# Performance work log

Hardware: AMD Instinct MI355X
Metric: run time of the kernel (lower is better)

The kernel has to match this reference:

```python
import jax, jax.numpy as jnp
import numpy as np

N_HEAD = 12


def setup_inputs() -> dict:
    key = jax.random.key(0)
    k1, k2, k3 = jax.random.split(key, 3)
    B, T, C = 1, 4096, 768
    x = jax.random.normal(k1, (B, T, C), dtype=jnp.float32)
    w_attn = jax.random.normal(k2, (C, 3 * C), dtype=jnp.float32) * (1.0 / np.sqrt(C))
    w_proj = jax.random.normal(k3, (C, C), dtype=jnp.float32) * (1.0 / np.sqrt(C))
    return {"x": x, "w_attn": w_attn, "w_proj": w_proj}


def reference(x, w_attn, w_proj):
    B, T, C = x.shape
    hd = C // N_HEAD
    qkv = x @ w_attn  # [B, T, 3C]
    q, k, v = jnp.split(qkv, 3, axis=-1)
    # [B, H, T, hd]
    q = q.reshape(B, T, N_HEAD, hd).transpose(0, 2, 1, 3)
    k = k.reshape(B, T, N_HEAD, hd).transpose(0, 2, 1, 3)
    v = v.reshape(B, T, N_HEAD, hd).transpose(0, 2, 1, 3)
    scale = 1.0 / np.sqrt(hd).astype(np.float32)
    att = jnp.einsum('bhtd,bhsd->bhts', q, k) * scale  # materialized TxT scores
    causal = jnp.tril(jnp.ones((T, T), dtype=bool))
    att = jnp.where(causal[None, None], att, -jnp.inf)
    att = jax.nn.softmax(att, axis=-1)
    y = jnp.einsum('bhts,bhsd->bhtd', att, v)  # [B, H, T, hd]
    y = y.transpose(0, 2, 1, 3).reshape(B, T, C)
    return y @ w_proj
```

## Files before the change

### kernel.cpp

```cpp
#include <hip/hip_runtime.h>


typedef short bf16x8 __attribute__((ext_vector_type(8)));
typedef float f32x4 __attribute__((ext_vector_type(4)));

#define T_SEQ 4096
#define C_DIM 768
#define NH 12
#define HD 64

__device__ __forceinline__ unsigned short f2bf(float f) {
  union { float f; unsigned u; } v; v.f = f;
  unsigned r = v.u + 0x7FFFu + ((v.u >> 16) & 1u);
  return (unsigned short)(r >> 16);
}
__device__ __forceinline__ float bf2f(unsigned short u) {
  union { unsigned u; float f; } v; v.u = ((unsigned)u) << 16;
  return v.f;
}
__device__ __forceinline__ unsigned cvtpk(float a, float b) {
  unsigned r;
  asm("v_cvt_pk_bf16_f32 %0, %1, %2" : "=v"(r) : "v"(a), "v"(b));
  return r;
}
#define E2(x) __builtin_amdgcn_exp2f(x)

#define GLD16(g, l) __builtin_amdgcn_global_load_lds( \
    (const __attribute__((address_space(1))) void*)(g), \
    (__attribute__((address_space(3))) void*)(l), 16, 0, 0)

__device__ __forceinline__ void tr_body(const float* __restrict__ in,
                                        unsigned short* __restrict__ out,
                                        int R, int Cc, int bx, int by,
                                        float (*tile)[33]) {
  int tx = threadIdx.x & 31, ty = threadIdx.x >> 5;
#pragma unroll
  for (int i = 0; i < 32; i += 8)
    tile[ty + i][tx] = in[(size_t)(by * 32 + ty + i) * Cc + bx * 32 + tx];
  __syncthreads();
#pragma unroll
  for (int i = 0; i < 32; i += 8)
    out[(size_t)(bx * 32 + ty + i) * R + by * 32 + tx] = f2bf(tile[tx][ty + i]);
}

__global__ void prep(const float* __restrict__ x, unsigned short* __restrict__ Xb,
                     const float* __restrict__ w_attn, unsigned short* __restrict__ WaT,
                     const float* __restrict__ w_proj, unsigned short* __restrict__ WpT) {
  __shared__ float tile[32][33];
  const int bid = blockIdx.x;
  if (bid < 3072) {
    int i = (bid * 256 + threadIdx.x) * 4;
    float4 v = *reinterpret_cast<const float4*>(x + i);
    ushort4 o;
    o.x = f2bf(v.x); o.y = f2bf(v.y); o.z = f2bf(v.z); o.w = f2bf(v.w);
    *reinterpret_cast<ushort4*>(Xb + i) = o;
  } else if (bid < 3072 + 1728) {
    int b = bid - 3072;
    tr_body(w_attn, WaT, 768, 2304, b % 72, b / 72, tile);
  } else {
    int b = bid - 4800;
    tr_body(w_proj, WpT, 768, 768, b % 24, b / 24, tile);
  }
}

template <int MODE>
__global__ __launch_bounds__(256, 4)
void gemm_bt(const unsigned short* __restrict__ A,
             const unsigned short* __restrict__ Bt,
             void* __restrict__ out0,
             unsigned short* __restrict__ Kout,
             unsigned short* __restrict__ Vt,
             int M, int N, int K) {
  __shared__ __align__(16) unsigned short As[128 * 64];
  __shared__ __align__(16) unsigned short Bs[64 * 64];
  const int nbn = N / 64;
  const int nwg = (M / 128) * nbn;
  const int cpx = nwg >> 3;
  const int swz = ((int)blockIdx.x & 7) * cpx + ((int)blockIdx.x >> 3);
  const int bm = swz / nbn, bn = swz % nbn;
  const int tid = threadIdx.x;
  const int wid = tid >> 6, lane = tid & 63;
  const int wr = wid >> 1, wc = wid & 1;
  const int lr = lane & 15;
  const int lk8 = (lane >> 4) * 8;
  const int rsub = lane >> 3, csub = (lane & 7) * 8;

  f32x4 acc[4][2] = {};

  const int nk = K / 64;
  for (int kt = 0; kt < nk; ++kt) {
    __syncthreads();
    {
      const unsigned short* gA = A + (size_t)(bm * 128) * K + kt * 64;
      const unsigned short* gB = Bt + (size_t)(bn * 64) * K + kt * 64;
#pragma unroll
      for (int c = 0; c < 4; ++c) {
        int seg = wid * 4 + c;
        int row = seg * 8 + rsub;
        GLD16(gA + (size_t)row * K + csub, (char*)As + seg * 1024);
      }
#pragma unroll
      for (int c = 0; c < 2; ++c) {
        int seg = wid * 2 + c;
        int row = seg * 8 + rsub;
        GLD16(gB + (size_t)row * K + csub, (char*)Bs + seg * 1024);
      }
    }
    __syncthreads();
#pragma unroll
    for (int kk = 0; kk < 2; ++kk) {
      bf16x8 a[4], b[2];
      int lk = kk * 32 + lk8;
#pragma unroll
      for (int m = 0; m < 4; ++m)
        a[m] = *reinterpret_cast<const bf16x8*>(&As[(wr * 64 + m * 16 + lr) * 64 + lk]);
#pragma unroll
      for (int n = 0; n < 2; ++n)
        b[n] = *reinterpret_cast<const bf16x8*>(&Bs[(wc * 32 + n * 16 + lr) * 64 + lk]);
#pragma unroll
      for (int m = 0; m < 4; ++m)
#pragma unroll
        for (int n = 0; n < 2; ++n)
          acc[m][n] = __builtin_amdgcn_mfma_f32_16x16x32_bf16(a[m], b[n], acc[m][n], 0, 0, 0);
    }
  }

  const int row0 = bm * 128 + wr * 64;
  const int col0 = bn * 64 + wc * 32;
#pragma unroll
  for (int m = 0; m < 4; ++m)
#pragma unroll
    for (int n = 0; n < 2; ++n)
#pragma unroll
      for (int j = 0; j < 4; ++j) {
        int r = row0 + m * 16 + (lane >> 4) * 4 + j;
        int c = col0 + n * 16 + (lane & 15);
        float v = acc[m][n][j];
        if (MODE == 0) {
          if (c < 768)
            ((unsigned short*)out0)[(size_t)r * 768 + c] = f2bf(v * 0.180336884f);
          else if (c < 1536)
            Kout[(size_t)r * 768 + (c - 768)] = f2bf(v);
          else
            Vt[(size_t)(c - 1536) * M + r] = f2bf(v);
        } else {
          ((float*)out0)[(size_t)r * N + c] = v;
        }
      }
}

__device__ __forceinline__ void stage_kv(const unsigned short* __restrict__ Kb,
                                         const unsigned short* __restrict__ Vt,
                                         unsigned short* Kbuf, unsigned short* Vbuf,
                                         int h, int st, int wid, int lane) {
  const int cg = lane & 7, rsub = (lane >> 3) & 7;
  const unsigned short* gK = Kb + (size_t)(st * 64) * C_DIM + h * 64;
  const unsigned short* gV = Vt + (size_t)(h * 64) * T_SEQ + st * 64;
#pragma unroll
  for (int c = 0; c < 2; ++c) {
    int seg = wid * 2 + c;
    int row = seg * 8 + rsub;
    GLD16(gK + (size_t)row * C_DIM + (cg ^ rsub) * 8, (char*)Kbuf + seg * 1024);
    GLD16(gV + (size_t)row * T_SEQ + (cg ^ rsub) * 8, (char*)Vbuf + seg * 1024);
  }
}

__device__ __forceinline__ int nchunks(int q) { return (2 * q + 13) / 12; }
__device__ __forceinline__ int part_off(int qb) {
  if (qb < 12) return (qb - 6) * 2;
  if (qb < 18) return 12 + (qb - 12) * 3;
  if (qb < 24) return 30 + (qb - 18) * 4;
  if (qb < 30) return 54 + (qb - 24) * 5;
  return 84 + (qb - 30) * 6;
}
__device__ __forceinline__ unsigned short* part_ptr(char* pA, char* pB, int set) {
  return (set < 768) ? (unsigned short*)(pA + (size_t)set * 16384)
                     : (unsigned short*)(pB + (size_t)(set - 768) * 16384);
}

__global__ __launch_bounds__(256, 3)
void attn_fwd(const unsigned short* __restrict__ Qb,
              const unsigned short* __restrict__ Kb,
              const unsigned short* __restrict__ Vt,
              unsigned short* __restrict__ Y,
              char* __restrict__ partA, char* __restrict__ partB,
              float* __restrict__ ml) {
  __shared__ __align__(16) unsigned short Ks[2][64 * 64];
  __shared__ __align__(16) unsigned short Vs[2][64 * 64];
  __shared__ __align__(16) unsigned short Ps[4][32 * 64];

  const int h = blockIdx.x;
  int qb = 0, ck = 0;
  {
    int idx = blockIdx.y;
    for (int q = 31; q >= 0; --q) {
      int nc = nchunks(q);
      if (idx < nc) { qb = q; ck = idx; break; }
      idx -= nc;
    }
  }
  const int nch = nchunks(qb);
  const int q0 = qb * 128;
  const int nst_total = 2 * qb + 2;
  const int st0 = ck * 12;
  const int st1 = (st0 + 12 < nst_total) ? st0 + 12 : nst_total;

  const int tid = threadIdx.x;
  const int wid = tid >> 6, lane = tid & 63;
  const int l15 = lane & 15, g = lane >> 4;
  const int sw = l15 & 7;
  const int qw = q0 + wid * 32;

  bf16x8 qf[2][2];
#pragma unroll
  for (int m = 0; m < 2; ++m)
#pragma unroll
    for (int kk = 0; kk < 2; ++kk)
      qf[m][kk] = *reinterpret_cast<const bf16x8*>(
          &Qb[(size_t)(qw + m * 16 + l15) * C_DIM + h * 64 + kk * 32 + g * 8]);

  f32x4 o[2][4] = {};
  float mrow[2] = {-1e30f, -1e30f};
  float lsum[2] = {0.f, 0.f};

  stage_kv(Kb, Vt, Ks[0], Vs[0], h, st0, wid, lane);
  int cur = 0;

  for (int st = st0; st < st1; ++st) {
    if (st + 1 < st1) {
      stage_kv(Kb, Vt, Ks[cur ^ 1], Vs[cur ^ 1], h, st + 1, wid, lane);
      asm volatile("s_waitcnt vmcnt(4)" ::: "memory");
    } else {
      asm volatile("s_waitcnt vmcnt(0)" ::: "memory");
    }
    __builtin_amdgcn_s_barrier();

    const bool active = (st * 64) <= (qw + 31);
    if (active) {
      const unsigned short* K_ = Ks[cur];
      const unsigned short* V_ = Vs[cur];

      f32x4 sT[2][4] = {};
      __builtin_amdgcn_s_setprio(1);
#pragma unroll
      for (int kk = 0; kk < 2; ++kk) {
        bf16x8 kf[4];
#pragma unroll
        for (int n = 0; n < 4; ++n)
          kf[n] = *reinterpret_cast<const bf16x8*>(
              &K_[(n * 16 + l15) * 64 + (((kk * 4 + g) ^ sw) * 8)]);
#pragma unroll
        for (int m = 0; m < 2; ++m)
#pragma unroll
          for (int n = 0; n < 4; ++n)
            sT[m][n] = __builtin_amdgcn_mfma_f32_16x16x32_bf16(kf[n], qf[m][kk], sT[m][n], 0, 0, 0);
      }
      __builtin_amdgcn_s_setprio(0);

      unsigned short* Pw = Ps[wid];
#pragma unroll
      for (int m = 0; m < 2; ++m) {
        if (!(st * 64 + 63 <= qw + m * 16)) {
          const int bound = (qw + m * 16 + l15) - st * 64;
#pragma unroll
          for (int n = 0; n < 4; ++n)
#pragma unroll
            for (int jj = 0; jj < 4; ++jj) {
              int sl = n * 16 + g * 4 + jj;
              if (sl > bound) sT[m][n][jj] = -1e30f;
            }
        }
        float vm[4];
#pragma unroll
        for (int n = 0; n < 4; ++n)
          vm[n] = fmaxf(fmaxf(sT[m][n][0], sT[m][n][1]), fmaxf(sT[m][n][2], sT[m][n][3]));
        float vmax = fmaxf(fmaxf(vm[0], vm[1]), fmaxf(vm[2], vm[3]));
        vmax = fmaxf(vmax, __shfl_xor(vmax, 16, 64));
        vmax = fmaxf(vmax, __shfl_xor(vmax, 32, 64));
        const bool defer = (__all(vmax <= mrow[m] + 8.0f) != 0);
        const float mnew = defer ? mrow[m] : fmaxf(mrow[m], vmax);
#pragma unroll
        for (int n = 0; n < 4; ++n)
#pragma unroll
          for (int jj = 0; jj < 4; ++jj)
            sT[m][n][jj] = E2(sT[m][n][jj] - mnew);
        float sm[4];
#pragma unroll
        for (int n = 0; n < 4; ++n)
          sm[n] = (sT[m][n][0] + sT[m][n][1]) + (sT[m][n][2] + sT[m][n][3]);
        float ps = (sm[0] + sm[1]) + (sm[2] + sm[3]);
        ps += __shfl_xor(ps, 16, 64);
        ps += __shfl_xor(ps, 32, 64);
        if (defer) {
          lsum[m] += ps;
        } else {
          float alpha = E2(mrow[m] - mnew);
          lsum[m] = lsum[m] * alpha + ps;
          mrow[m] = mnew;
#pragma unroll
          for (int n2 = 0; n2 < 4; ++n2) o[m][n2] *= alpha;
        }
#pragma unroll
        for (int n = 0; n < 4; ++n) {
          uint2 pw;
          pw.x = cvtpk(sT[m][n][0], sT[m][n][1]);
          pw.y = cvtpk(sT[m][n][2], sT[m][n][3]);
          *reinterpret_cast<uint2*>(
              &Pw[(m * 16 + l15) * 64 + (((n * 2 + (g >> 1)) ^ sw) * 8) + (g & 1) * 4]) = pw;
        }
      }
      asm volatile("s_waitcnt lgkmcnt(0)" ::: "memory");

      __builtin_amdgcn_s_setprio(1);
#pragma unroll
      for (int ks = 0; ks < 2; ++ks) {
        bf16x8 vf[4], pf[2];
#pragma unroll
        for (int n2 = 0; n2 < 4; ++n2)
          vf[n2] = *reinterpret_cast<const bf16x8*>(
              &V_[(n2 * 16 + l15) * 64 + (((ks * 4 + g) ^ sw) * 8)]);
#pragma unroll
        for (int m = 0; m < 2; ++m)
          pf[m] = *reinterpret_cast<const bf16x8*>(
              &Pw[(m * 16 + l15) * 64 + (((ks * 4 + g) ^ sw) * 8)]);
#pragma unroll
        for (int m = 0; m < 2; ++m)
#pragma unroll
          for (int n2 = 0; n2 < 4; ++n2)
            o[m][n2] = __builtin_amdgcn_mfma_f32_16x16x32_bf16(vf[n2], pf[m], o[m][n2], 0, 0, 0);
      }
      __builtin_amdgcn_s_setprio(0);
    }
    asm volatile("" ::: "memory");
    __builtin_amdgcn_s_barrier();
    cur ^= 1;
  }

  if (nch == 1) {
#pragma unroll
    for (int m = 0; m < 2; ++m) {
      float inv = 1.0f / lsum[m];
      int qg = qw + m * 16 + l15;
#pragma unroll
      for (int n2 = 0; n2 < 4; ++n2) {
        uint2 yk;
        yk.x = cvtpk(o[m][n2][0] * inv, o[m][n2][1] * inv);
        yk.y = cvtpk(o[m][n2][2] * inv, o[m][n2][3] * inv);
        *reinterpret_cast<uint2*>(&Y[(size_t)qg * C_DIM + h * 64 + n2 * 16 + g * 4]) = yk;
      }
    }
  } else {
    const int set = h * 96 + part_off(qb) + ck;
    unsigned short* po = part_ptr(partA, partB, set);
#pragma unroll
    for (int m = 0; m < 2; ++m) {
      int qL = wid * 32 + m * 16 + l15;
#pragma unroll
      for (int n2 = 0; n2 < 4; ++n2) {
        uint2 pk;
        pk.x = cvtpk(o[m][n2][0], o[m][n2][1]);
        pk.y = cvtpk(o[m][n2][2], o[m][n2][3]);
        *reinterpret_cast<uint2*>(&po[qL * 64 + n2 * 16 + g * 4]) = pk;
      }
      if (g == 0) {
        ml[(size_t)set * 256 + qL * 2] = mrow[m];
        ml[(size_t)set * 256 + qL * 2 + 1] = lsum[m];
      }
    }
  }
}

__global__ __launch_bounds__(256)
void attn_combine(char* __restrict__ partA, char* __restrict__ partB,
                  const float* __restrict__ ml, unsigned short* __restrict__ Y) {
  const int qb = 6 + blockIdx.x;
  const int h = blockIdx.y;
  const int nch = nchunks(qb);
  const int set0 = h * 96 + part_off(qb);
  const int t = threadIdx.x;
  const int r = t >> 1, dh = (t & 1) * 32;

  float mi[6], li[6];
  float M = -1e30f;
  for (int i = 0; i < nch; ++i) {
    mi[i] = ml[(size_t)(set0 + i) * 256 + r * 2];
    li[i] = ml[(size_t)(set0 + i) * 256 + r * 2 + 1];
    M = fmaxf(M, mi[i]);
  }
  float L = 0.f;
  float O[32];
#pragma unroll
  for (int d = 0; d < 32; ++d) O[d] = 0.f;
  for (int i = 0; i < nch; ++i) {
    float w = E2(mi[i] - M);
    L += li[i] * w;
    const unsigned short* po = part_ptr(partA, partB, set0 + i) + r * 64 + dh;
#pragma unroll
    for (int d4 = 0; d4 < 32; d4 += 4) {
      ushort4 v = *reinterpret_cast<const ushort4*>(po + d4);
      O[d4 + 0] += bf2f(v.x) * w;
      O[d4 + 1] += bf2f(v.y) * w;
      O[d4 + 2] += bf2f(v.z) * w;
      O[d4 + 3] += bf2f(v.w) * w;
    }
  }
  float inv = 1.0f / L;
  unsigned short* yp = Y + (size_t)(qb * 128 + r) * C_DIM + h * 64 + dh;
#pragma unroll
  for (int d4 = 0; d4 < 32; d4 += 4) {
    uint2 yk;
    yk.x = cvtpk(O[d4 + 0] * inv, O[d4 + 1] * inv);
    yk.y = cvtpk(O[d4 + 2] * inv, O[d4 + 3] * inv);
    *reinterpret_cast<uint2*>(yp + d4) = yk;
  }
}

extern "C" void kernel_launch(void* const* d_in, const int* in_sizes, int n_in,
                              void* d_out, int out_size, void* d_ws, size_t ws_size,
                              hipStream_t stream) {
  const float* x = (const float*)d_in[0];
  const float* w_attn = (const float*)d_in[1];
  const float* w_proj = (const float*)d_in[2];
  float* out = (float*)d_out;

  char* ws = (char*)d_ws;
  unsigned short* Xb   = (unsigned short*)(ws + 0);
  unsigned short* WaT  = (unsigned short*)(ws + 6291456);
  unsigned short* WpT  = (unsigned short*)(ws + 9830400);
  unsigned short* Qb   = (unsigned short*)(ws + 11010048);
  unsigned short* Kb   = (unsigned short*)(ws + 17301504);
  unsigned short* Vt   = (unsigned short*)(ws + 23592960);
  unsigned short* Yb   = (unsigned short*)(ws + 29884416);

  char* partA = (char*)d_out;
  char* partB = (char*)ws;
  float* mlp  = (float*)(ws + 6291456);

  prep<<<5376, 256, 0, stream>>>(x, Xb, w_attn, WaT, w_proj, WpT);

  gemm_bt<0><<<(T_SEQ / 128) * (2304 / 64), 256, 0, stream>>>(
      Xb, WaT, (void*)Qb, Kb, Vt, T_SEQ, 2304, C_DIM);

  attn_fwd<<<dim3(NH, 102), 256, 0, stream>>>(Qb, Kb, Vt, Yb, partA, partB, mlp);
  attn_combine<<<dim3(26, NH), 256, 0, stream>>>(partA, partB, mlp, Yb);

  gemm_bt<1><<<(T_SEQ / 128) * (C_DIM / 64), 256, 0, stream>>>(
      Yb, WpT, (void*)out, nullptr, nullptr, T_SEQ, C_DIM, C_DIM);
}
```

Before: 138.1 us.

## Single-buffer V tile in attention and shrink output-projection GEMM tile

The attention kernel now double-buffers only K, keeps one V buffer, and issues the next V load after the end-of-iteration barrier. This cuts LDS use, which may allow more resident workgroups. In exchange, the V load has less time to arrive before the PV MFMAs need it. The GEMM is templated on tile size, and the output projection uses 64x64 tiles to launch twice as many workgroups, trading per-block reuse for better occupancy across the CUs.

```diff
diff --git a/kernel.cpp b/kernel.cpp
--- a/kernel.cpp
+++ b/kernel.cpp
@@ -63,7 +63,7 @@
   }
 }
 
-template <int MODE>
+template <int MODE, int BM, int BN>
 __global__ __launch_bounds__(256, 4)
 void gemm_bt(const unsigned short* __restrict__ A,
              const unsigned short* __restrict__ Bt,
@@ -71,10 +71,11 @@
              unsigned short* __restrict__ Kout,
              unsigned short* __restrict__ Vt,
              int M, int N, int K) {
-  __shared__ __align__(16) unsigned short As[128 * 64];
-  __shared__ __align__(16) unsigned short Bs[64 * 64];
-  const int nbn = N / 64;
-  const int nwg = (M / 128) * nbn;
+  __shared__ __align__(16) unsigned short As[BM * 64];
+  __shared__ __align__(16) unsigned short Bs[BN * 64];
+  constexpr int AM = BM / 32, AN = BN / 32;
+  const int nbn = N / BN;
+  const int nwg = (M / BM) * nbn;
   const int cpx = nwg >> 3;
   const int swz = ((int)blockIdx.x & 7) * cpx + ((int)blockIdx.x >> 3);
   const int bm = swz / nbn, bn = swz % nbn;
@@ -85,23 +86,23 @@
   const int lk8 = (lane >> 4) * 8;
   const int rsub = lane >> 3, csub = (lane & 7) * 8;
 
-  f32x4 acc[4][2] = {};
+  f32x4 acc[AM][AN] = {};
 
   const int nk = K / 64;
   for (int kt = 0; kt < nk; ++kt) {
     __syncthreads();
     {
-      const unsigned short* gA = A + (size_t)(bm * 128) * K + kt * 64;
-      const unsigned short* gB = Bt + (size_t)(bn * 64) * K + kt * 64;
-#pragma unroll
-      for (int c = 0; c < 4; ++c) {
-        int seg = wid * 4 + c;
+      const unsigned short* gA = A + (size_t)(bm * BM) * K + kt * 64;
+      const unsigned short* gB = Bt + (size_t)(bn * BN) * K + kt * 64;
+#pragma unroll
+      for (int c = 0; c < BM / 32; ++c) {
+        int seg = wid * (BM / 32) + c;
         int row = seg * 8 + rsub;
         GLD16(gA + (size_t)row * K + csub, (char*)As + seg * 1024);
       }
 #pragma unroll
-      for (int c = 0; c < 2; ++c) {
-        int seg = wid * 2 + c;
+      for (int c = 0; c < BN / 32; ++c) {
+        int seg = wid * (BN / 32) + c;
         int row = seg * 8 + rsub;
         GLD16(gB + (size_t)row * K + csub, (char*)Bs + seg * 1024);
       }
@@ -109,28 +110,28 @@
     __syncthreads();
 #pragma unroll
     for (int kk = 0; kk < 2; ++kk) {
-      bf16x8 a[4], b[2];
+      bf16x8 a[AM], b[AN];
       int lk = kk * 32 + lk8;
 #pragma unroll
-      for (int m = 0; m < 4; ++m)
-        a[m] = *reinterpret_cast<const bf16x8*>(&As[(wr * 64 + m * 16 + lr) * 64 + lk]);
-#pragma unroll
-      for (int n = 0; n < 2; ++n)
-        b[n] = *reinterpret_cast<const bf16x8*>(&Bs[(wc * 32 + n * 16 + lr) * 64 + lk]);
-#pragma unroll
-      for (int m = 0; m < 4; ++m)
-#pragma unroll
-        for (int n = 0; n < 2; ++n)
+      for (int m = 0; m < AM; ++m)
+        a[m] = *reinterpret_cast<const bf16x8*>(&As[(wr * (BM / 2) + m * 16 + lr) * 64 + lk]);
+#pragma unroll
+      for (int n = 0; n < AN; ++n)
+        b[n] = *reinterpret_cast<const bf16x8*>(&Bs[(wc * (BN / 2) + n * 16 + lr) * 64 + lk]);
+#pragma unroll
+      for (int m = 0; m < AM; ++m)
+#pragma unroll
+        for (int n = 0; n < AN; ++n)
           acc[m][n] = __builtin_amdgcn_mfma_f32_16x16x32_bf16(a[m], b[n], acc[m][n], 0, 0, 0);
     }
   }
 
-  const int row0 = bm * 128 + wr * 64;
-  const int col0 = bn * 64 + wc * 32;
-#pragma unroll
-  for (int m = 0; m < 4; ++m)
-#pragma unroll
-    for (int n = 0; n < 2; ++n)
+  const int row0 = bm * BM + wr * (BM / 2);
+  const int col0 = bn * BN + wc * (BN / 2);
+#pragma unroll
+  for (int m = 0; m < AM; ++m)
+#pragma unroll
+    for (int n = 0; n < AN; ++n)
 #pragma unroll
       for (int j = 0; j < 4; ++j) {
         int r = row0 + m * 16 + (lane >> 4) * 4 + j;
@@ -149,18 +150,27 @@
       }
 }
 
-__device__ __forceinline__ void stage_kv(const unsigned short* __restrict__ Kb,
-                                         const unsigned short* __restrict__ Vt,
-                                         unsigned short* Kbuf, unsigned short* Vbuf,
-                                         int h, int st, int wid, int lane) {
+__device__ __forceinline__ void stage_k(const unsigned short* __restrict__ Kb,
+                                        unsigned short* Kbuf,
+                                        int h, int st, int wid, int lane) {
   const int cg = lane & 7, rsub = (lane >> 3) & 7;
   const unsigned short* gK = Kb + (size_t)(st * 64) * C_DIM + h * 64;
-  const unsigned short* gV = Vt + (size_t)(h * 64) * T_SEQ + st * 64;
 #pragma unroll
   for (int c = 0; c < 2; ++c) {
     int seg = wid * 2 + c;
     int row = seg * 8 + rsub;
     GLD16(gK + (size_t)row * C_DIM + (cg ^ rsub) * 8, (char*)Kbuf + seg * 1024);
+  }
+}
+__device__ __forceinline__ void stage_v(const unsigned short* __restrict__ Vt,
+                                        unsigned short* Vbuf,
+                                        int h, int st, int wid, int lane) {
+  const int cg = lane & 7, rsub = (lane >> 3) & 7;
+  const unsigned short* gV = Vt + (size_t)(h * 64) * T_SEQ + st * 64;
+#pragma unroll
+  for (int c = 0; c < 2; ++c) {
+    int seg = wid * 2 + c;
+    int row = seg * 8 + rsub;
     GLD16(gV + (size_t)row * T_SEQ + (cg ^ rsub) * 8, (char*)Vbuf + seg * 1024);
   }
 }
@@ -186,7 +196,7 @@
               char* __restrict__ partA, char* __restrict__ partB,
               float* __restrict__ ml) {
   __shared__ __align__(16) unsigned short Ks[2][64 * 64];
-  __shared__ __align__(16) unsigned short Vs[2][64 * 64];
+  __shared__ __align__(16) unsigned short Vs[64 * 64];
   __shared__ __align__(16) unsigned short Ps[4][32 * 64];
 
   const int h = blockIdx.x;
@@ -223,13 +233,15 @@
   float mrow[2] = {-1e30f, -1e30f};
   float lsum[2] = {0.f, 0.f};
 
-  stage_kv(Kb, Vt, Ks[0], Vs[0], h, st0, wid, lane);
+  stage_k(Kb, Ks[0], h, st0, wid, lane);
+  stage_v(Vt, Vs, h, st0, wid, lane);
   int cur = 0;
 
   for (int st = st0; st < st1; ++st) {
-    if (st + 1 < st1) {
-      stage_kv(Kb, Vt, Ks[cur ^ 1], Vs[cur ^ 1], h, st + 1, wid, lane);
-      asm volatile("s_waitcnt vmcnt(4)" ::: "memory");
+    const bool haveNext = (st + 1 < st1);
+    if (haveNext) {
+      stage_k(Kb, Ks[cur ^ 1], h, st + 1, wid, lane);
+      asm volatile("s_waitcnt vmcnt(2)" ::: "memory");
     } else {
       asm volatile("s_waitcnt vmcnt(0)" ::: "memory");
     }
@@ -238,7 +250,6 @@
     const bool active = (st * 64) <= (qw + 31);
     if (active) {
       const unsigned short* K_ = Ks[cur];
-      const unsigned short* V_ = Vs[cur];
 
       f32x4 sT[2][4] = {};
       __builtin_amdgcn_s_setprio(1);
@@ -318,7 +329,7 @@
 #pragma unroll
         for (int n2 = 0; n2 < 4; ++n2)
           vf[n2] = *reinterpret_cast<const bf16x8*>(
-              &V_[(n2 * 16 + l15) * 64 + (((ks * 4 + g) ^ sw) * 8)]);
+              &Vs[(n2 * 16 + l15) * 64 + (((ks * 4 + g) ^ sw) * 8)]);
 #pragma unroll
         for (int m = 0; m < 2; ++m)
           pf[m] = *reinterpret_cast<const bf16x8*>(
@@ -333,6 +344,7 @@
     }
     asm volatile("" ::: "memory");
     __builtin_amdgcn_s_barrier();
+    if (haveNext) stage_v(Vt, Vs, h, st + 1, wid, lane);
     cur ^= 1;
   }
 
@@ -438,12 +450,12 @@
 
   prep<<<5376, 256, 0, stream>>>(x, Xb, w_attn, WaT, w_proj, WpT);
 
-  gemm_bt<0><<<(T_SEQ / 128) * (2304 / 64), 256, 0, stream>>>(
+  gemm_bt<0, 128, 64><<<(T_SEQ / 128) * (2304 / 64), 256, 0, stream>>>(
       Xb, WaT, (void*)Qb, Kb, Vt, T_SEQ, 2304, C_DIM);
 
   attn_fwd<<<dim3(NH, 102), 256, 0, stream>>>(Qb, Kb, Vt, Yb, partA, partB, mlp);
   attn_combine<<<dim3(26, NH), 256, 0, stream>>>(partA, partB, mlp, Yb);
 
-  gemm_bt<1><<<(T_SEQ / 128) * (C_DIM / 64), 256, 0, stream>>>(
+  gemm_bt<1, 64, 64><<<(T_SEQ / 64) * (C_DIM / 64), 256, 0, stream>>>(
       Yb, WpT, (void*)out, nullptr, nullptr, T_SEQ, C_DIM, C_DIM);
 }
```

Measured after the change: 137.8 us. About the same (-0.2%).
